# Kernel tuning notes

Hardware: AMD Instinct MI355X
Metric: run time of the kernel (lower is better)

The kernel has to match this reference:

```python
import jax, jax.numpy as jnp
import numpy as np
from jax import lax

THR = 1.0
SLOPE = 25.0
EPS = 1e-5

@jax.custom_vjp
def spike(u):
    # Heaviside with fast-sigmoid surrogate gradient (slope=25)
    return (u > 0.0).astype(u.dtype)

def _spike_fwd(u):
    return (u > 0.0).astype(u.dtype), u

def _spike_bwd(u, g):
    return (g / (SLOPE * jnp.abs(u) + 1.0) ** 2,)

spike.defvjp(_spike_fwd, _spike_bwd)

def lif_scan(inp, beta):
    # inp: (T, B, H); snntorch Leaky, reset_mechanism='subtract', init mem=0
    def step(mem, cur):
        reset = lax.stop_gradient(spike(mem - THR))
        mem = beta * mem + cur - reset * THR
        spk = spike(mem - THR)
        return mem, (spk, mem)
    mem0 = jnp.zeros(inp.shape[1:], inp.dtype)
    _, (spk, mem) = lax.scan(step, mem0, inp)
    return spk, mem

def bn_per_step(h, g, b):
    # h: (T, B, H); training-mode BatchNorm1d applied per timestep over batch
    m = h.mean(axis=1, keepdims=True)
    v = h.var(axis=1, keepdims=True)
    return (h - m) / jnp.sqrt(v + EPS) * g + b

def setup_inputs() -> dict:
    key = jax.random.key(0)
    ks = jax.random.split(key, 16)
    B, T, C = 128, 128, 32
    H, Ts, HOR, K = 512, 4, 96, 3
    s = 0.02
    return {
        "x": jax.random.normal(ks[0], (B, T, C), jnp.float32),
        "conv_w": jax.random.normal(ks[1], (H * Ts, C, K), jnp.float32) * s,
        "conv_b": jnp.zeros((H * Ts,), jnp.float32),
        "bn1_g": jnp.ones((H * Ts,), jnp.float32),
        "bn1_b": jnp.zeros((H * Ts,), jnp.float32),
        "beta_enc": jnp.full((H,), 0.9, jnp.float32),
        "bn2_g": jnp.ones((H,), jnp.float32),
        "bn2_b": jnp.zeros((H,), jnp.float32),
        "beta2": jnp.full((H,), 0.9, jnp.float32),
        "bn3_g": jnp.ones((H,), jnp.float32),
        "bn3_b": jnp.zeros((H,), jnp.float32),
        "beta3": jnp.full((H,), 0.9, jnp.float32),
        "wq": jax.random.normal(ks[2], (H, H), jnp.float32) * s,
        "bq": jnp.zeros((H,), jnp.float32),
        "wk": jax.random.normal(ks[3], (H, H), jnp.float32) * s,
        "bk": jnp.zeros((H,), jnp.float32),
        "wv": jax.random.normal(ks[4], (H, H), jnp.float32) * s,
        "bv": jnp.zeros((H,), jnp.float32),
        "bna_g": jnp.ones((H,), jnp.float32),
        "bna_b": jnp.zeros((H,), jnp.float32),
        "wh": jax.random.normal(ks[5], (HOR, H), jnp.float32) * s,
        "bh": jnp.zeros((HOR,), jnp.float32),
    }

def reference(x, conv_w, conv_b, bn1_g, bn1_b, beta_enc, bn2_g, bn2_b, beta2,
              bn3_g, bn3_b, beta3, wq, bq, wk, bk, wv, bv, bna_g, bna_b, wh, bh):
    B, T, C = x.shape
    H = beta2.shape[0]
    Ts = conv_w.shape[0] // H
    # Conv spike encoder: Conv1d(C -> H*Ts, k, pad=k//2)
    k = conv_w.shape[2]
    h = lax.conv_general_dilated(x.transpose(0, 2, 1), conv_w, (1,), [(k // 2, k // 2)],
                                 dimension_numbers=("NCH", "OIH", "NCH"))
    h = h + conv_b[None, :, None]  # (B, H*Ts, T)
    # BatchNorm1d (training mode): stats over (B, T) per channel, biased var
    m = h.mean((0, 2), keepdims=True)
    v = h.var((0, 2), keepdims=True)
    h = (h - m) / jnp.sqrt(v + EPS) * bn1_g[None, :, None] + bn1_b[None, :, None]
    # (B, H*Ts, T) -> (T*Ts, B, H)
    h = h.transpose(0, 2, 1).reshape(B, T, Ts, H).reshape(B, T * Ts, H).transpose(1, 0, 2)
    spk_enc, _ = lif_scan(h, jnp.clip(beta_enc, 0.0, 0.99))
    # bn2 -> lif2 -> bn3 -> lif3 (BN applied per step in the torch loop)
    h2 = bn_per_step(spk_enc, bn2_g, bn2_b)
    s2, _ = lif_scan(h2, jnp.clip(beta2, 0.0, 0.99))
    h3 = bn_per_step(s2, bn3_g, bn3_b)
    _, mem3 = lif_scan(h3, jnp.clip(beta3, 0.0, 0.99))  # (Ttot, B, H)
    # Spiking attention over membrane trajectory
    xa = mem3.transpose(1, 0, 2)  # (B, Ttot, H)
    Q = xa @ wq.T + bq
    K = xa @ wk.T + bk
    V = xa @ wv.T + bv
    attn = jax.nn.sigmoid(jnp.einsum("btd,bsd->bts", Q, K) * (H ** -0.5))
    feat = jnp.einsum("bts,bsd->btd", attn, V).mean(axis=1)  # (B, H)
    mf = feat.mean(0, keepdims=True)
    vf = feat.var(0, keepdims=True)
    feat = (feat - mf) / jnp.sqrt(vf + EPS) * bna_g + bna_b
    return feat @ wh.T + bh  # (B, horizon)
```

## Files before the change

### kernel.cpp

```cpp
#include <hip/hip_runtime.h>
#include <math.h>

#define EPSF 1e-5f

static constexpr int Bn   = 128;
static constexpr int Tn   = 128;
static constexpr int Cn   = 32;
static constexpr int On   = 2048;
static constexpr int Hn   = 512;
static constexpr int TTn  = 512;
static constexpr int HORn = 96;
static constexpr int BH   = Bn * Hn;
static constexpr float THRf = 1.0f;

__device__ __forceinline__ float bf2f(unsigned short u) {
    union { unsigned int i; float f; } v; v.i = ((unsigned int)u) << 16; return v.f;
}
__device__ __forceinline__ unsigned short f2bf(float f) {
    union { float f; unsigned int i; } v; v.f = f;
    unsigned int r = v.i + 0x7fff + ((v.i >> 16) & 1);
    return (unsigned short)(r >> 16);
}

using bfrag  = __attribute__((ext_vector_type(8))) short;
using f32x4v = __attribute__((ext_vector_type(4))) float;
using us8v   = __attribute__((ext_vector_type(8))) unsigned short;

#define GLD16(gp, lp) __builtin_amdgcn_global_load_lds( \
    (const __attribute__((address_space(1))) void*)(gp), \
    (__attribute__((address_space(3))) void*)(lp), 16, 0, 0)

__global__ __launch_bounds__(256) void im2col_k(const float* __restrict__ x,
    unsigned short* __restrict__ Ph, unsigned short* __restrict__ Pl)
{
    int idx = blockIdx.x * 256 + threadIdx.x;
    int row = idx / 96, kc = idx - row * 96;
    int k = kc >> 5, c = kc & 31;
    int t = row & 127, b = row >> 7;
    int tg = t + k - 1;
    float v = (tg >= 0 && tg < Tn) ? x[((size_t)b * Tn + tg) * Cn + c] : 0.f;
    unsigned short hi = f2bf(v);
    Ph[idx] = hi;
    Pl[idx] = f2bf(v - bf2f(hi));
}

__global__ __launch_bounds__(256) void wprep_k(const float* __restrict__ wconv,
    unsigned short* __restrict__ Wh, unsigned short* __restrict__ Wl)
{
    int idx = blockIdx.x * 256 + threadIdx.x;
    int o = idx / 96, kc = idx - o * 96;
    int k = kc >> 5, c = kc & 31;
    float v = wconv[(size_t)o * 96 + c * 3 + k];
    unsigned short hi = f2bf(v);
    Wh[idx] = hi;
    Wl[idx] = f2bf(v - bf2f(hi));
}

__global__ __launch_bounds__(256) void conv_mfma_k(
    const unsigned short* __restrict__ Ph, const unsigned short* __restrict__ Pl,
    const unsigned short* __restrict__ Wh, const unsigned short* __restrict__ Wl,
    float* __restrict__ raw, float* __restrict__ sums)
{
    const int b  = blockIdx.x;
    const int n0 = blockIdx.y * 128;
    const int tid = threadIdx.x;
    const int lane = tid & 63;
    const int quad = lane >> 4, lr = lane & 15;
    const int wid = tid >> 6, wm = wid & 1, wn = wid >> 1;

    f32x4v acc[4][4] = {};
#pragma unroll
    for (int ks = 0; ks < 3; ks++) {
        const int col = ks * 32 + quad * 8;
        bfrag ah[4], al[4], bh[4], bl[4];
#pragma unroll
        for (int mi = 0; mi < 4; mi++) {
            size_t roff = ((size_t)b * 128 + wm * 64 + mi * 16 + lr) * 96 + col;
            ah[mi] = *(const bfrag*)(Ph + roff);
            al[mi] = *(const bfrag*)(Pl + roff);
        }
#pragma unroll
        for (int ni = 0; ni < 4; ni++) {
            size_t roff = (size_t)(n0 + wn * 64 + ni * 16 + lr) * 96 + col;
            bh[ni] = *(const bfrag*)(Wh + roff);
            bl[ni] = *(const bfrag*)(Wl + roff);
        }
#pragma unroll
        for (int mi = 0; mi < 4; mi++)
#pragma unroll
            for (int ni = 0; ni < 4; ni++) {
                acc[mi][ni] = __builtin_amdgcn_mfma_f32_16x16x32_bf16(
                    ah[mi], bh[ni], acc[mi][ni], 0, 0, 0);
                acc[mi][ni] = __builtin_amdgcn_mfma_f32_16x16x32_bf16(
                    ah[mi], bl[ni], acc[mi][ni], 0, 0, 0);
                acc[mi][ni] = __builtin_amdgcn_mfma_f32_16x16x32_bf16(
                    al[mi], bh[ni], acc[mi][ni], 0, 0, 0);
            }
    }
#pragma unroll
    for (int ni = 0; ni < 4; ni++) {
        int o = n0 + wn * 64 + ni * 16 + lr;
        int ts = o >> 9, hh = o & 511;
        float s = 0.f, ss = 0.f;
#pragma unroll
        for (int mi = 0; mi < 4; mi++)
#pragma unroll
            for (int r = 0; r < 4; r++) {
                int t = wm * 64 + mi * 16 + quad * 4 + r;
                float v = acc[mi][ni][r];
                raw[((size_t)(t * 4 + ts) * Bn + b) * Hn + hh] = v;
                s += v; ss += v * v;
            }
        s  += __shfl_xor(s, 16);  s  += __shfl_xor(s, 32);
        ss += __shfl_xor(ss, 16); ss += __shfl_xor(ss, 32);
        if (quad == 0) {
            atomicAdd(&sums[o], s);
            atomicAdd(&sums[On + o], ss);
        }
    }
}

__global__ void bn1_final_k(const float* __restrict__ sums,
                            const float* __restrict__ g, const float* __restrict__ bb,
                            float* __restrict__ scale, float* __restrict__ shift)
{
    int o = blockIdx.x * 256 + threadIdx.x;
    float m = sums[o] * (1.f / 16384.f);
    float v = sums[On + o] * (1.f / 16384.f) - m * m;
    float sc = g[o] / sqrtf(v + EPSF);
    scale[o] = sc;
    shift[o] = bb[o] - m * sc;
}

__global__ __launch_bounds__(256) void lif1_k(const float* __restrict__ raw,
    const float* __restrict__ scale, const float* __restrict__ shift,
    const float* __restrict__ beta_in, unsigned char* __restrict__ spk)
{
    const int thr = blockIdx.x * 256 + threadIdx.x;
    const int hh = thr & 511;
    const float beta = fminf(fmaxf(beta_in[hh], 0.f), 0.99f);
    float sc[4], sh[4];
#pragma unroll
    for (int ts = 0; ts < 4; ts++) { sc[ts] = scale[ts * Hn + hh]; sh[ts] = shift[ts * Hn + hh]; }
    float mem = 0.f;
    for (int tt = 0; tt < TTn; tt += 8) {
        float cu[8];
#pragma unroll
        for (int u = 0; u < 8; u++) cu[u] = raw[(size_t)(tt + u) * BH + thr];
#pragma unroll
        for (int u = 0; u < 8; u++) {
            float cur = cu[u] * sc[u & 3] + sh[u & 3];
            float reset = mem > THRf ? 1.f : 0.f;
            mem = beta * mem + cur - reset;
            spk[(size_t)(tt + u) * BH + thr] = mem > THRf ? (unsigned char)1 : (unsigned char)0;
        }
    }
}

__global__ __launch_bounds__(256) void bnstep_k(const unsigned char* __restrict__ spk,
    const float* __restrict__ g, const float* __restrict__ bb,
    float* __restrict__ av, float* __restrict__ zv)
{
    const int tt = blockIdx.x;
    const int h0 = threadIdx.x * 2;
    int c0 = 0, c1 = 0;
    const unsigned char* base = spk + (size_t)tt * BH + h0;
#pragma unroll 8
    for (int b = 0; b < Bn; b++) {
        unsigned short v = *(const unsigned short*)(base + (size_t)b * Hn);
        c0 += (v & 0xff); c1 += (v >> 8);
    }
#pragma unroll
    for (int q = 0; q < 2; q++) {
        int hh = h0 + q;
        float p = (q ? c1 : c0) * (1.f / 128.f);
        float inv = 1.f / sqrtf(p - p * p + EPSF);
        float gi = g[hh] * inv;
        float zz = bb[hh] - p * gi;
        av[(size_t)tt * Hn + hh] = gi + zz;
        zv[(size_t)tt * Hn + hh] = zz;
    }
}

__global__ __launch_bounds__(256) void lif2_k(const unsigned char* __restrict__ sin_,
    const float* __restrict__ av, const float* __restrict__ zv,
    const float* __restrict__ beta_in, unsigned char* __restrict__ sout)
{
    const int thr = blockIdx.x * 256 + threadIdx.x;
    const int hh = thr & 511;
    const float beta = fminf(fmaxf(beta_in[hh], 0.f), 0.99f);
    float mem = 0.f;
    for (int tt = 0; tt < TTn; tt += 8) {
        float aa[8], zz[8]; unsigned char ss[8];
#pragma unroll
        for (int u = 0; u < 8; u++) {
            ss[u] = sin_[(size_t)(tt + u) * BH + thr];
            aa[u] = av[(size_t)(tt + u) * Hn + hh];
            zz[u] = zv[(size_t)(tt + u) * Hn + hh];
        }
#pragma unroll
        for (int u = 0; u < 8; u++) {
            float cur = ss[u] ? aa[u] : zz[u];
            float reset = mem > THRf ? 1.f : 0.f;
            mem = beta * mem + cur - reset;
            sout[(size_t)(tt + u) * BH + thr] = mem > THRf ? (unsigned char)1 : (unsigned char)0;
        }
    }
}

__global__ __launch_bounds__(256) void lif3_k(const unsigned char* __restrict__ sin_,
    const float* __restrict__ av, const float* __restrict__ zv,
    const float* __restrict__ beta_in, unsigned short* __restrict__ mem3b)
{
    const int thr = blockIdx.x * 256 + threadIdx.x;
    const int hh = thr & 511;
    const int b = thr >> 9;
    const float beta = fminf(fmaxf(beta_in[hh], 0.f), 0.99f);
    float mem = 0.f;
    for (int tt = 0; tt < TTn; tt += 8) {
        float aa[8], zz[8]; unsigned char ss[8];
#pragma unroll
        for (int u = 0; u < 8; u++) {
            ss[u] = sin_[(size_t)(tt + u) * BH + thr];
            aa[u] = av[(size_t)(tt + u) * Hn + hh];
            zz[u] = zv[(size_t)(tt + u) * Hn + hh];
        }
#pragma unroll
        for (int u = 0; u < 8; u++) {
            float cur = ss[u] ? aa[u] : zz[u];
            float reset = mem > THRf ? 1.f : 0.f;
            mem = beta * mem + cur - reset;
            mem3b[((size_t)b * TTn + (tt + u)) * Hn + hh] = f2bf(mem);
        }
    }
}

__global__ __launch_bounds__(256) void gemm_atb_k(const float* __restrict__ Aw,
    const float* __restrict__ Bw, float* __restrict__ GTp)
{
    __shared__ float As[8][132];
    __shared__ float Bs[8][132];
    const int m0 = blockIdx.x * 128;
    const int n0 = blockIdx.y * 128;
    const int kz = blockIdx.z;
    const int tid = threadIdx.x;
    const int ir = tid >> 5, cl = (tid & 31) * 4;
    const float* Ap = Aw + (size_t)ir * 512 + m0 + cl;
    const float* Bp = Bw + (size_t)ir * 512 + n0 + cl;
    const int tm = tid & 15, tn = tid >> 4;
    float acc[8][8];
#pragma unroll
    for (int i = 0; i < 8; i++)
#pragma unroll
        for (int j = 0; j < 8; j++) acc[i][j] = 0.f;

    for (int i0 = kz * 64; i0 < kz * 64 + 64; i0 += 8) {
        const float4 avv = *(const float4*)(Ap + (size_t)i0 * 512);
        const float4 bvv = *(const float4*)(Bp + (size_t)i0 * 512);
        __syncthreads();
        *(float4*)&As[ir][cl] = avv;
        *(float4*)&Bs[ir][cl] = bvv;
        __syncthreads();
#pragma unroll
        for (int kk = 0; kk < 8; kk++) {
            float4 a0 = *(const float4*)&As[kk][tm * 8];
            float4 a1 = *(const float4*)&As[kk][tm * 8 + 4];
            float4 b0 = *(const float4*)&Bs[kk][tn * 8];
            float4 b1 = *(const float4*)&Bs[kk][tn * 8 + 4];
            float a_[8] = {a0.x, a0.y, a0.z, a0.w, a1.x, a1.y, a1.z, a1.w};
            float b_[8] = {b0.x, b0.y, b0.z, b0.w, b1.x, b1.y, b1.z, b1.w};
#pragma unroll
            for (int i = 0; i < 8; i++)
#pragma unroll
                for (int j = 0; j < 8; j++) acc[i][j] += a_[i] * b_[j];
        }
    }
    float* outp = GTp + (size_t)kz * Hn * Hn;
#pragma unroll
    for (int i = 0; i < 8; i++) {
        size_t rowoff = (size_t)(m0 + tm * 8 + i) * 512 + n0 + tn * 8;
#pragma unroll
        for (int j = 0; j < 8; j++) outp[rowoff + j] = acc[i][j];
    }
}

__global__ void gtred_k(const float* __restrict__ GTp, unsigned short* __restrict__ GT)
{
    int idx = blockIdx.x * 256 + threadIdx.x;
    float s = 0.f;
#pragma unroll
    for (int z = 0; z < 8; z++) s += GTp[(size_t)z * Hn * Hn + idx];
    GT[idx] = f2bf(s);
}

__global__ __launch_bounds__(256) void bias_prep_k(const float* __restrict__ wq,
    const float* __restrict__ wk, const float* __restrict__ bq,
    const float* __restrict__ bk, float* __restrict__ qb, float* __restrict__ kb)
{
    const int blk = blockIdx.x;
    const bool doq = blk < 8;
    const int d0 = (doq ? blk : blk - 8) * 64;
    const float* W    = doq ? wq : wk;
    const float* bvec = doq ? bk : bq;
    const int dl = threadIdx.x & 63, ig = threadIdx.x >> 6;
    float s = 0.f;
    for (int i = ig * 128; i < ig * 128 + 128; i++)
        s += W[(size_t)i * 512 + d0 + dl] * bvec[i];
    __shared__ float red[4][64];
    red[ig][dl] = s;
    __syncthreads();
    if (ig == 0)
        (doq ? qb : kb)[d0 + dl] = red[0][dl] + red[1][dl] + red[2][dl] + red[3][dl];
}

__global__ void c0_k(const float* __restrict__ bq, const float* __restrict__ bk,
                     float* __restrict__ c0)
{
    __shared__ float red[256];
    float p = 0.f;
    for (int i = threadIdx.x; i < 512; i += 256) p += bq[i] * bk[i];
    red[threadIdx.x] = p;
    __syncthreads();
    for (int s = 128; s > 0; s >>= 1) {
        if (threadIdx.x < s) red[threadIdx.x] += red[threadIdx.x + s];
        __syncthreads();
    }
    if (threadIdx.x == 0) c0[0] = red[0];
}

__global__ __launch_bounds__(256) void ygemm_k(const unsigned short* __restrict__ A,
    const unsigned short* __restrict__ Bsrc, const float* __restrict__ qb,
    const float* __restrict__ kb, const float* __restrict__ c0,
    unsigned short* __restrict__ C, float* __restrict__ rowq,
    float* __restrict__ rowk)
{
    __shared__ unsigned short As[128 * 64];
    __shared__ unsigned short Bs[128 * 64];
    const int m0 = blockIdx.x * 128;
    const int n0 = blockIdx.y * 128;
    const int tid = threadIdx.x;
    const int lane = tid & 63;
    const int quad = lane >> 4, lr = lane & 15;
    const int wid = tid >> 6;
    const int wm = wid & 1, wn = wid >> 1;

    const int srw = lane >> 3;
    const int scc = (lane & 7) ^ (srw & 7);
    const unsigned short* gA = A    + (size_t)(m0 + wid * 32 + srw) * 512 + scc * 8;
    const unsigned short* gB = Bsrc + (size_t)(n0 + wid * 32 + srw) * 512 + scc * 8;

    const bool dorows = (blockIdx.y == 0) && (wn == 0);
    float rq_acc[4] = {0.f, 0.f, 0.f, 0.f};
    float rk_acc[4] = {0.f, 0.f, 0.f, 0.f};

    f32x4v acc[4][4] = {};
    for (int k0 = 0; k0 < 512; k0 += 64) {
        __syncthreads();
#pragma unroll
        for (int j = 0; j < 4; j++) {
            GLD16(gA + (size_t)j * 8 * 512 + k0, As + (wid * 32 + j * 8) * 64);
            GLD16(gB + (size_t)j * 8 * 512 + k0, Bs + (wid * 32 + j * 8) * 64);
        }
        __syncthreads();
#pragma unroll
        for (int kk = 0; kk < 2; kk++) {
            const int slot = (kk * 4 + quad) ^ (lr & 7);
            bfrag af[4], bf_[4];
#pragma unroll
            for (int mi = 0; mi < 4; mi++)
                af[mi] = *(const bfrag*)&As[(wm * 64 + mi * 16 + lr) * 64 + slot * 8];
#pragma unroll
            for (int ni = 0; ni < 4; ni++)
                bf_[ni] = *(const bfrag*)&Bs[(wn * 64 + ni * 16 + lr) * 64 + slot * 8];
#pragma unroll
            for (int mi = 0; mi < 4; mi++)
#pragma unroll
                for (int ni = 0; ni < 4; ni++)
                    acc[mi][ni] = __builtin_amdgcn_mfma_f32_16x16x32_bf16(
                        af[mi], bf_[ni], acc[mi][ni], 0, 0, 0);
            if (dorows) {
                const int koff = k0 + kk * 32 + quad * 8;
                const float4 qv0 = *(const float4*)(qb + koff);
                const float4 qv1 = *(const float4*)(qb + koff + 4);
                const float4 kv0 = *(const float4*)(kb + koff);
                const float4 kv1 = *(const float4*)(kb + koff + 4);
                const float qv[8] = {qv0.x, qv0.y, qv0.z, qv0.w, qv1.x, qv1.y, qv1.z, qv1.w};
                const float kv[8] = {kv0.x, kv0.y, kv0.z, kv0.w, kv1.x, kv1.y, kv1.z, kv1.w};
#pragma unroll
                for (int mi = 0; mi < 4; mi++)
#pragma unroll
                    for (int j = 0; j < 8; j++) {
                        float a = bf2f((unsigned short)af[mi][j]);
                        rq_acc[mi] += a * qv[j];
                        rk_acc[mi] += a * kv[j];
                    }
            }
        }
    }
#pragma unroll
    for (int mi = 0; mi < 4; mi++)
#pragma unroll
        for (int ni = 0; ni < 4; ni++) {
            int col = n0 + wn * 64 + ni * 16 + lr;
#pragma unroll
            for (int r = 0; r < 4; r++) {
                int row = m0 + wm * 64 + mi * 16 + quad * 4 + r;
                C[(size_t)row * 512 + col] = f2bf(acc[mi][ni][r]);
            }
        }
    if (dorows) {
        const float c0v = c0[0];
#pragma unroll
        for (int mi = 0; mi < 4; mi++) {
            float rq = rq_acc[mi], rk = rk_acc[mi];
            rq += __shfl_xor(rq, 16); rq += __shfl_xor(rq, 32);
            rk += __shfl_xor(rk, 16); rk += __shfl_xor(rk, 32);
            if (quad == 0) {
                int row = m0 + wm * 64 + mi * 16 + lr;
                rowq[row] = rq + c0v;
                rowk[row] = rk;
            }
        }
    }
}

__global__ __launch_bounds__(256) void scores_k(const unsigned short* __restrict__ Y,
    const unsigned short* __restrict__ Xm, const float* __restrict__ rowq,
    const float* __restrict__ rowk, float* __restrict__ wacc)
{
    __shared__ unsigned short As[128 * 64];
    __shared__ unsigned short Bs[128 * 64];
    __shared__ float colsum[128];
    __shared__ float rq_s[128], rk_s[128];
    const int b  = blockIdx.z;
    const int m0 = blockIdx.x * 128;
    const int n0 = blockIdx.y * 128;
    const int tid = threadIdx.x;
    const int lane = tid & 63;
    const int quad = lane >> 4, lr = lane & 15;
    const int wid = tid >> 6;
    const int wm = wid & 1, wn = wid >> 1;

    if (tid < 128) {
        colsum[tid] = 0.f;
        rq_s[tid] = rowq[(size_t)b * TTn + m0 + tid];
        rk_s[tid] = rowk[(size_t)b * TTn + n0 + tid];
    }

    const int srw = lane >> 3;
    const int scc = (lane & 7) ^ (srw & 7);
    const unsigned short* gA = Y  + (size_t)b * TTn * Hn
        + (size_t)(m0 + wid * 32 + srw) * 512 + scc * 8;
    const unsigned short* gB = Xm + (size_t)b * TTn * Hn
        + (size_t)(n0 + wid * 32 + srw) * 512 + scc * 8;

    f32x4v acc[4][4] = {};
    for (int k0 = 0; k0 < 512; k0 += 64) {
        __syncthreads();
#pragma unroll
        for (int j = 0; j < 4; j++) {
            GLD16(gA + (size_t)j * 8 * 512 + k0, As + (wid * 32 + j * 8) * 64);
            GLD16(gB + (size_t)j * 8 * 512 + k0, Bs + (wid * 32 + j * 8) * 64);
        }
        __syncthreads();
#pragma unroll
        for (int kk = 0; kk < 2; kk++) {
            const int slot = (kk * 4 + quad) ^ (lr & 7);
            bfrag af[4], bf_[4];
#pragma unroll
            for (int mi = 0; mi < 4; mi++)
                af[mi] = *(const bfrag*)&As[(wm * 64 + mi * 16 + lr) * 64 + slot * 8];
#pragma unroll
            for (int ni = 0; ni < 4; ni++)
                bf_[ni] = *(const bfrag*)&Bs[(wn * 64 + ni * 16 + lr) * 64 + slot * 8];
#pragma unroll
            for (int mi = 0; mi < 4; mi++)
#pragma unroll
                for (int ni = 0; ni < 4; ni++)
                    acc[mi][ni] = __builtin_amdgcn_mfma_f32_16x16x32_bf16(
                        af[mi], bf_[ni], acc[mi][ni], 0, 0, 0);
        }
    }
    const float scl = 0.044194173824159216f;
#pragma unroll
    for (int ni = 0; ni < 4; ni++) {
        float s_ln = 0.f;
        float rkv = rk_s[wn * 64 + ni * 16 + lr];
#pragma unroll
        for (int mi = 0; mi < 4; mi++) {
#pragma unroll
            for (int r = 0; r < 4; r++) {
                float rqv = rq_s[wm * 64 + mi * 16 + quad * 4 + r];
                float xv = (acc[mi][ni][r] + rqv + rkv) * scl;
                s_ln += 1.f / (1.f + __expf(-xv));
            }
        }
        atomicAdd(&colsum[wn * 64 + ni * 16 + lr], s_ln);
    }
    __syncthreads();
    if (tid < 128)
        atomicAdd(&wacc[(size_t)b * TTn + n0 + tid], colsum[tid] * (1.f / 512.f));
}

__global__ __launch_bounds__(256) void wsum_k(const float* __restrict__ wacc,
    const unsigned short* __restrict__ mem3b, float* __restrict__ u,
    float* __restrict__ W1)
{
    const int b = blockIdx.x;
    const int tid = threadIdx.x;
    __shared__ float ws_[512];
    __shared__ float red[256];
    ws_[tid] = wacc[(size_t)b * TTn + tid];
    ws_[tid + 256] = wacc[(size_t)b * TTn + tid + 256];
    __syncthreads();
    red[tid] = ws_[tid] + ws_[tid + 256];
    __syncthreads();
    for (int s = 128; s > 0; s >>= 1) {
        if (tid < s) red[tid] += red[tid + s];
        __syncthreads();
    }
    if (tid == 0) W1[b] = red[0];
    float a0 = 0.f, a1 = 0.f;
    const unsigned short* Xb = mem3b + (size_t)b * TTn * Hn;
    for (int s = 0; s < TTn; s++) {
        float w = ws_[s];
        a0 += w * bf2f(Xb[(size_t)s * Hn + tid]);
        a1 += w * bf2f(Xb[(size_t)s * Hn + tid + 256]);
    }
    u[(size_t)b * Hn + tid] = a0;
    u[(size_t)b * Hn + tid + 256] = a1;
}

__global__ __launch_bounds__(256) void feat2_k(const float* __restrict__ u,
    const float* __restrict__ W1, const float* __restrict__ wv,
    const float* __restrict__ bv, float* __restrict__ feat)
{
    const int b = blockIdx.x;
    const int tid = threadIdx.x;
    __shared__ float us[512];
    us[tid] = u[(size_t)b * Hn + tid];
    us[tid + 256] = u[(size_t)b * Hn + tid + 256];
    __syncthreads();
    const float w1 = W1[b];
#pragma unroll
    for (int q = 0; q < 2; q++) {
        int d = tid + q * 256;
        float acc = bv[d] * w1;
        const float* wr = wv + (size_t)d * 512;
        for (int e = 0; e < 512; e += 4) {
            float4 w4 = *(const float4*)(wr + e);
            acc += us[e] * w4.x + us[e+1] * w4.y + us[e+2] * w4.z + us[e+3] * w4.w;
        }
        feat[(size_t)b * Hn + d] = acc;
    }
}

__global__ void bna_k(const float* __restrict__ feat, const float* __restrict__ g,
                      const float* __restrict__ bb, float* __restrict__ featn)
{
    int d = blockIdx.x * 256 + threadIdx.x;
    float s = 0.f, ss = 0.f;
    for (int b = 0; b < Bn; b++) { float v = feat[(size_t)b * Hn + d]; s += v; ss += v * v; }
    float m = s * (1.f / 128.f);
    float var = ss * (1.f / 128.f) - m * m;
    float sc = g[d] / sqrtf(var + EPSF);
    float sh = bb[d] - m * sc;
    for (int b = 0; b < Bn; b++) featn[(size_t)b * Hn + d] = feat[(size_t)b * Hn + d] * sc + sh;
}

__global__ __launch_bounds__(128) void head_k(const float* __restrict__ featn,
    const float* __restrict__ wh, const float* __restrict__ bh, float* __restrict__ out)
{
    const int b = blockIdx.x;
    __shared__ float f[512];
    const int tid = threadIdx.x;
    for (int i = tid; i < 512; i += 128) f[i] = featn[(size_t)b * Hn + i];
    __syncthreads();
    if (tid < HORn) {
        float accv = bh[tid];
        const float* wr = wh + (size_t)tid * Hn;
        for (int d = 0; d < 512; d++) accv += f[d] * wr[d];
        out[(size_t)b * HORn + tid] = accv;
    }
}

__global__ void dbg_k(float* out, float v) { out[0] = v; }

extern "C" void kernel_launch(void* const* d_in, const int* in_sizes, int n_in,
                              void* d_out, int out_size, void* d_ws, size_t ws_size,
                              hipStream_t stream)
{
    (void)in_sizes; (void)n_in;
    const float* x      = (const float*)d_in[0];
    const float* conv_w = (const float*)d_in[1];
    const float* bn1_g  = (const float*)d_in[3];
    const float* bn1_b  = (const float*)d_in[4];
    const float* beta_e = (const float*)d_in[5];
    const float* bn2_g  = (const float*)d_in[6];
    const float* bn2_b  = (const float*)d_in[7];
    const float* beta2  = (const float*)d_in[8];
    const float* bn3_g  = (const float*)d_in[9];
    const float* bn3_b  = (const float*)d_in[10];
    const float* beta3  = (const float*)d_in[11];
    const float* wq     = (const float*)d_in[12];
    const float* bq     = (const float*)d_in[13];
    const float* wk     = (const float*)d_in[14];
    const float* bk     = (const float*)d_in[15];
    const float* wv     = (const float*)d_in[16];
    const float* bv     = (const float*)d_in[17];
    const float* bna_g  = (const float*)d_in[18];
    const float* bna_b  = (const float*)d_in[19];
    const float* wh     = (const float*)d_in[20];
    const float* bh     = (const float*)d_in[21];
    float* out = (float*)d_out;

    char* ws = (char*)d_ws;
    size_t off = 0;
    auto alloc = [&](size_t bytes) {
        char* p = ws + off;
        off += (bytes + 255) & ~(size_t)255;
        return p;
    };
    float* raw          = (float*)alloc((size_t)TTn * BH * 4);
    unsigned char* spk1 = (unsigned char*)alloc((size_t)TTn * BH);
    unsigned char* s2   = (unsigned char*)alloc((size_t)TTn * BH);
    unsigned short* Ph = (unsigned short*)alloc((size_t)Bn * Tn * 96 * 2);
    unsigned short* Pl = (unsigned short*)alloc((size_t)Bn * Tn * 96 * 2);
    unsigned short* Wh = (unsigned short*)alloc((size_t)On * 96 * 2);
    unsigned short* Wl = (unsigned short*)alloc((size_t)On * 96 * 2);
    float* sums   = (float*)alloc(2 * On * 4);
    float* scale1 = (float*)alloc(On * 4);
    float* shift1 = (float*)alloc(On * 4);
    float* a2     = (float*)alloc((size_t)TTn * Hn * 4);
    float* z2     = (float*)alloc((size_t)TTn * Hn * 4);
    float* a3     = (float*)alloc((size_t)TTn * Hn * 4);
    float* z3     = (float*)alloc((size_t)TTn * Hn * 4);
    float* wacc   = (float*)alloc((size_t)Bn * TTn * 4);
    float* GTp    = (float*)alloc((size_t)8 * Hn * Hn * 4);
    unsigned short* GT = (unsigned short*)alloc((size_t)Hn * Hn * 2);
    float* qb     = (float*)alloc(Hn * 4);
    float* kb     = (float*)alloc(Hn * 4);
    float* c0     = (float*)alloc(256);
    float* rowq   = (float*)alloc((size_t)Bn * TTn * 4);
    float* rowk   = (float*)alloc((size_t)Bn * TTn * 4);
    float* u      = (float*)alloc((size_t)Bn * Hn * 4);
    float* W1     = (float*)alloc(Bn * 4);
    float* feat   = (float*)alloc((size_t)Bn * Hn * 4);
    float* featn  = (float*)alloc((size_t)Bn * Hn * 4);
    unsigned short* mem3b = (unsigned short*)raw;
    unsigned short* Y     = (unsigned short*)spk1;

    if (ws_size < off) {
        hipMemsetAsync(d_out, 0, (size_t)out_size * 4, stream);
        dbg_k<<<1, 1, 0, stream>>>(out, (float)ws_size);
        return;
    }

    hipMemsetAsync(sums, 0, 2 * On * 4, stream);
    hipMemsetAsync(wacc, 0, (size_t)Bn * TTn * 4, stream);

    im2col_k<<<(Bn * Tn * 96) / 256, 256, 0, stream>>>(x, Ph, Pl);
    wprep_k<<<(On * 96) / 256, 256, 0, stream>>>(conv_w, Wh, Wl);
    conv_mfma_k<<<dim3(Bn, On / 128), 256, 0, stream>>>(Ph, Pl, Wh, Wl, raw, sums);
    bn1_final_k<<<On / 256, 256, 0, stream>>>(sums, bn1_g, bn1_b, scale1, shift1);
    lif1_k<<<BH / 256, 256, 0, stream>>>(raw, scale1, shift1, beta_e, spk1);
    bnstep_k<<<TTn, 256, 0, stream>>>(spk1, bn2_g, bn2_b, a2, z2);
    lif2_k<<<BH / 256, 256, 0, stream>>>(spk1, a2, z2, beta2, s2);
    bnstep_k<<<TTn, 256, 0, stream>>>(s2, bn3_g, bn3_b, a3, z3);
    lif3_k<<<BH / 256, 256, 0, stream>>>(s2, a3, z3, beta3, mem3b);
    gemm_atb_k<<<dim3(4, 4, 8), 256, 0, stream>>>(wk, wq, GTp);
    gtred_k<<<(Hn * Hn) / 256, 256, 0, stream>>>(GTp, GT);
    bias_prep_k<<<16, 256, 0, stream>>>(wq, wk, bq, bk, qb, kb);
    c0_k<<<1, 256, 0, stream>>>(bq, bk, c0);
    ygemm_k<<<dim3((Bn * TTn) / 128, Hn / 128), 256, 0, stream>>>(
        mem3b, GT, qb, kb, c0, Y, rowq, rowk);
    scores_k<<<dim3(TTn / 128, TTn / 128, Bn), 256, 0, stream>>>(Y, mem3b, rowq, rowk, wacc);
    wsum_k<<<Bn, 256, 0, stream>>>(wacc, mem3b, u, W1);
    feat2_k<<<Bn, 256, 0, stream>>>(u, W1, wv, bv, feat);
    bna_k<<<Hn / 256, 256, 0, stream>>>(feat, bna_g, bna_b, featn);
    head_k<<<Bn, 128, 0, stream>>>(featn, wh, bh, out);
}
```

Before: 535.1 us.

## Switch attention GEMMs to 32x32x16 MFMA and vectorize weighted-sum kernel

The ygemm and scores kernels move from 16x16x32 bf16 MFMA tiles (4x4 per wave) to 32x32x16 tiles (2x2 per wave), with new LDS fragment indexing and output/epilogue mappings. This reduces LDS fragment reads per MFMA and uses the larger instruction shape. The wsum kernel now splits the time loop across 4 waves, each lane loading 8 bf16 values at once, then sums partial results in shared memory, replacing scalar 2-byte strided loads. The risks are extra shared memory and new accumulator layout bookkeeping that has to exactly match the 32x32 MFMA output format.

```diff
diff --git a/kernel.cpp b/kernel.cpp
--- a/kernel.cpp
+++ b/kernel.cpp
@@ -24,6 +24,7 @@
 
 using bfrag  = __attribute__((ext_vector_type(8))) short;
 using f32x4v = __attribute__((ext_vector_type(4))) float;
+using f32x16 = __attribute__((ext_vector_type(16))) float;
 using us8v   = __attribute__((ext_vector_type(8))) unsigned short;
 
 #define GLD16(gp, lp) __builtin_amdgcn_global_load_lds( \
@@ -340,7 +341,7 @@
     const int n0 = blockIdx.y * 128;
     const int tid = threadIdx.x;
     const int lane = tid & 63;
-    const int quad = lane >> 4, lr = lane & 15;
+    const int l31 = lane & 31, kw = lane >> 5;
     const int wid = tid >> 6;
     const int wm = wid & 1, wn = wid >> 1;
 
@@ -350,10 +351,10 @@
     const unsigned short* gB = Bsrc + (size_t)(n0 + wid * 32 + srw) * 512 + scc * 8;
 
     const bool dorows = (blockIdx.y == 0) && (wn == 0);
-    float rq_acc[4] = {0.f, 0.f, 0.f, 0.f};
-    float rk_acc[4] = {0.f, 0.f, 0.f, 0.f};
-
-    f32x4v acc[4][4] = {};
+    float rq_acc[2] = {0.f, 0.f};
+    float rk_acc[2] = {0.f, 0.f};
+
+    f32x16 acc[2][2] = {};
     for (int k0 = 0; k0 < 512; k0 += 64) {
         __syncthreads();
 #pragma unroll
@@ -363,23 +364,27 @@
         }
         __syncthreads();
 #pragma unroll
-        for (int kk = 0; kk < 2; kk++) {
-            const int slot = (kk * 4 + quad) ^ (lr & 7);
-            bfrag af[4], bf_[4];
-#pragma unroll
-            for (int mi = 0; mi < 4; mi++)
-                af[mi] = *(const bfrag*)&As[(wm * 64 + mi * 16 + lr) * 64 + slot * 8];
-#pragma unroll
-            for (int ni = 0; ni < 4; ni++)
-                bf_[ni] = *(const bfrag*)&Bs[(wn * 64 + ni * 16 + lr) * 64 + slot * 8];
-#pragma unroll
-            for (int mi = 0; mi < 4; mi++)
-#pragma unroll
-                for (int ni = 0; ni < 4; ni++)
-                    acc[mi][ni] = __builtin_amdgcn_mfma_f32_16x16x32_bf16(
+        for (int kk = 0; kk < 4; kk++) {
+            const int chunk = kk * 2 + kw;
+            bfrag af[2], bf_[2];
+#pragma unroll
+            for (int mi = 0; mi < 2; mi++) {
+                const int row = wm * 64 + mi * 32 + l31;
+                af[mi] = *(const bfrag*)&As[row * 64 + (chunk ^ (row & 7)) * 8];
+            }
+#pragma unroll
+            for (int ni = 0; ni < 2; ni++) {
+                const int row = wn * 64 + ni * 32 + l31;
+                bf_[ni] = *(const bfrag*)&Bs[row * 64 + (chunk ^ (row & 7)) * 8];
+            }
+#pragma unroll
+            for (int mi = 0; mi < 2; mi++)
+#pragma unroll
+                for (int ni = 0; ni < 2; ni++)
+                    acc[mi][ni] = __builtin_amdgcn_mfma_f32_32x32x16_bf16(
                         af[mi], bf_[ni], acc[mi][ni], 0, 0, 0);
             if (dorows) {
-                const int koff = k0 + kk * 32 + quad * 8;
+                const int koff = k0 + kk * 16 + kw * 8;
                 const float4 qv0 = *(const float4*)(qb + koff);
                 const float4 qv1 = *(const float4*)(qb + koff + 4);
                 const float4 kv0 = *(const float4*)(kb + koff);
@@ -387,7 +392,7 @@
                 const float qv[8] = {qv0.x, qv0.y, qv0.z, qv0.w, qv1.x, qv1.y, qv1.z, qv1.w};
                 const float kv[8] = {kv0.x, kv0.y, kv0.z, kv0.w, kv1.x, kv1.y, kv1.z, kv1.w};
 #pragma unroll
-                for (int mi = 0; mi < 4; mi++)
+                for (int mi = 0; mi < 2; mi++)
 #pragma unroll
                     for (int j = 0; j < 8; j++) {
                         float a = bf2f((unsigned short)af[mi][j]);
@@ -398,25 +403,26 @@
         }
     }
 #pragma unroll
-    for (int mi = 0; mi < 4; mi++)
-#pragma unroll
-        for (int ni = 0; ni < 4; ni++) {
-            int col = n0 + wn * 64 + ni * 16 + lr;
-#pragma unroll
-            for (int r = 0; r < 4; r++) {
-                int row = m0 + wm * 64 + mi * 16 + quad * 4 + r;
-                C[(size_t)row * 512 + col] = f2bf(acc[mi][ni][r]);
+    for (int mi = 0; mi < 2; mi++)
+#pragma unroll
+        for (int ni = 0; ni < 2; ni++) {
+            const int col = n0 + wn * 64 + ni * 32 + l31;
+#pragma unroll
+            for (int reg = 0; reg < 16; reg++) {
+                const int row = m0 + wm * 64 + mi * 32
+                              + (reg & 3) + 8 * (reg >> 2) + 4 * kw;
+                C[(size_t)row * 512 + col] = f2bf(acc[mi][ni][reg]);
             }
         }
     if (dorows) {
         const float c0v = c0[0];
 #pragma unroll
-        for (int mi = 0; mi < 4; mi++) {
+        for (int mi = 0; mi < 2; mi++) {
             float rq = rq_acc[mi], rk = rk_acc[mi];
-            rq += __shfl_xor(rq, 16); rq += __shfl_xor(rq, 32);
-            rk += __shfl_xor(rk, 16); rk += __shfl_xor(rk, 32);
-            if (quad == 0) {
-                int row = m0 + wm * 64 + mi * 16 + lr;
+            rq += __shfl_xor(rq, 32);
+            rk += __shfl_xor(rk, 32);
+            if (kw == 0) {
+                const int row = m0 + wm * 64 + mi * 32 + l31;
                 rowq[row] = rq + c0v;
                 rowk[row] = rk;
             }
@@ -437,7 +443,7 @@
     const int n0 = blockIdx.y * 128;
     const int tid = threadIdx.x;
     const int lane = tid & 63;
-    const int quad = lane >> 4, lr = lane & 15;
+    const int l31 = lane & 31, kw = lane >> 5;
     const int wid = tid >> 6;
     const int wm = wid & 1, wn = wid >> 1;
 
@@ -454,7 +460,7 @@
     const unsigned short* gB = Xm + (size_t)b * TTn * Hn
         + (size_t)(n0 + wid * 32 + srw) * 512 + scc * 8;
 
-    f32x4v acc[4][4] = {};
+    f32x16 acc[2][2] = {};
     for (int k0 = 0; k0 < 512; k0 += 64) {
         __syncthreads();
 #pragma unroll
@@ -464,38 +470,45 @@
         }
         __syncthreads();
 #pragma unroll
-        for (int kk = 0; kk < 2; kk++) {
-            const int slot = (kk * 4 + quad) ^ (lr & 7);
-            bfrag af[4], bf_[4];
-#pragma unroll
-            for (int mi = 0; mi < 4; mi++)
-                af[mi] = *(const bfrag*)&As[(wm * 64 + mi * 16 + lr) * 64 + slot * 8];
-#pragma unroll
-            for (int ni = 0; ni < 4; ni++)
-                bf_[ni] = *(const bfrag*)&Bs[(wn * 64 + ni * 16 + lr) * 64 + slot * 8];
-#pragma unroll
-            for (int mi = 0; mi < 4; mi++)
-#pragma unroll
-                for (int ni = 0; ni < 4; ni++)
-                    acc[mi][ni] = __builtin_amdgcn_mfma_f32_16x16x32_bf16(
+        for (int kk = 0; kk < 4; kk++) {
+            const int chunk = kk * 2 + kw;
+            bfrag af[2], bf_[2];
+#pragma unroll
+            for (int mi = 0; mi < 2; mi++) {
+                const int row = wm * 64 + mi * 32 + l31;
+                af[mi] = *(const bfrag*)&As[row * 64 + (chunk ^ (row & 7)) * 8];
+            }
+#pragma unroll
+            for (int ni = 0; ni < 2; ni++) {
+                const int row = wn * 64 + ni * 32 + l31;
+                bf_[ni] = *(const bfrag*)&Bs[row * 64 + (chunk ^ (row & 7)) * 8];
+            }
+#pragma unroll
+            for (int mi = 0; mi < 2; mi++)
+#pragma unroll
+                for (int ni = 0; ni < 2; ni++)
+                    acc[mi][ni] = __builtin_amdgcn_mfma_f32_32x32x16_bf16(
                         af[mi], bf_[ni], acc[mi][ni], 0, 0, 0);
         }
     }
     const float scl = 0.044194173824159216f;
 #pragma unroll
-    for (int ni = 0; ni < 4; ni++) {
+    for (int ni = 0; ni < 2; ni++) {
+        const int col_l = wn * 64 + ni * 32 + l31;
+        const float rkv = rk_s[col_l];
         float s_ln = 0.f;
-        float rkv = rk_s[wn * 64 + ni * 16 + lr];
-#pragma unroll
-        for (int mi = 0; mi < 4; mi++) {
-#pragma unroll
-            for (int r = 0; r < 4; r++) {
-                float rqv = rq_s[wm * 64 + mi * 16 + quad * 4 + r];
-                float xv = (acc[mi][ni][r] + rqv + rkv) * scl;
+#pragma unroll
+        for (int mi = 0; mi < 2; mi++) {
+#pragma unroll
+            for (int reg = 0; reg < 16; reg++) {
+                const int row_l = wm * 64 + mi * 32
+                                + (reg & 3) + 8 * (reg >> 2) + 4 * kw;
+                float xv = (acc[mi][ni][reg] + rq_s[row_l] + rkv) * scl;
                 s_ln += 1.f / (1.f + __expf(-xv));
             }
         }
-        atomicAdd(&colsum[wn * 64 + ni * 16 + lr], s_ln);
+        s_ln += __shfl_xor(s_ln, 32);
+        if (kw == 0) atomicAdd(&colsum[col_l], s_ln);
     }
     __syncthreads();
     if (tid < 128)
@@ -508,27 +521,37 @@
 {
     const int b = blockIdx.x;
     const int tid = threadIdx.x;
+    const int wid = tid >> 6, lane = tid & 63;
     __shared__ float ws_[512];
+    __shared__ float part[4][512];
     __shared__ float red[256];
     ws_[tid] = wacc[(size_t)b * TTn + tid];
     ws_[tid + 256] = wacc[(size_t)b * TTn + tid + 256];
     __syncthreads();
+    float a[8] = {0.f, 0.f, 0.f, 0.f, 0.f, 0.f, 0.f, 0.f};
+    const unsigned short* Xb = mem3b + (size_t)b * TTn * Hn + lane * 8;
+    for (int s = wid * 128; s < wid * 128 + 128; s++) {
+        const float w = ws_[s];
+        const us8v xv = *(const us8v*)(Xb + (size_t)s * Hn);
+#pragma unroll
+        for (int j = 0; j < 8; j++) a[j] += w * bf2f(xv[j]);
+    }
+#pragma unroll
+    for (int j = 0; j < 8; j++) part[wid][lane * 8 + j] = a[j];
     red[tid] = ws_[tid] + ws_[tid + 256];
     __syncthreads();
-    for (int s = 128; s > 0; s >>= 1) {
-        if (tid < s) red[tid] += red[tid + s];
+    for (int st = 128; st > 0; st >>= 1) {
+        if (tid < st) red[tid] += red[tid + st];
         __syncthreads();
     }
     if (tid == 0) W1[b] = red[0];
-    float a0 = 0.f, a1 = 0.f;
-    const unsigned short* Xb = mem3b + (size_t)b * TTn * Hn;
-    for (int s = 0; s < TTn; s++) {
-        float w = ws_[s];
-        a0 += w * bf2f(Xb[(size_t)s * Hn + tid]);
-        a1 += w * bf2f(Xb[(size_t)s * Hn + tid + 256]);
-    }
-    u[(size_t)b * Hn + tid] = a0;
-    u[(size_t)b * Hn + tid + 256] = a1;
+    if (wid == 0) {
+#pragma unroll
+        for (int j = 0; j < 8; j++) {
+            const int e = lane * 8 + j;
+            u[(size_t)b * Hn + e] = part[0][e] + part[1][e] + part[2][e] + part[3][e];
+        }
+    }
 }
 
 __global__ __launch_bounds__(256) void feat2_k(const float* __restrict__ u,
```

Result: faster. 500.9 us (-6.4%).
